# Performance work log

Measured on AMD Instinct MI355X. Metric: run time of the kernel, lower is better.

## Reference

```python
import jax, jax.numpy as jnp
import numpy as np

B, T, D, E = 4, 1024, 1024, 8
HD = 4 * D  # hdim = 4*dim


def setup_inputs() -> dict:
    key = jax.random.key(0)
    k1, k2, k3, k4 = jax.random.split(key, 4)
    std = 0.5 * D ** (-0.5)
    bound = (3.0 ** 0.5) * std
    x = jax.random.normal(k1, (B, T, D), dtype=jnp.float32)
    # router zero-init in source; use small random weights so routing is non-degenerate
    router_w = jax.random.normal(k2, (E, D), dtype=jnp.float32) * 0.02
    expert_fc = jax.random.uniform(k3, (E, D, HD), dtype=jnp.float32, minval=-bound, maxval=bound)
    # proj zero-init in source; use small random so output/backward are non-trivial
    expert_proj = jax.random.normal(k4, (E, D, HD), dtype=jnp.float32) * 0.02
    return {"x": x, "router_w": router_w, "expert_fc": expert_fc, "expert_proj": expert_proj}


def reference(x, router_w, expert_fc, expert_proj):
    # router: Linear(dim, E, bias=False) -> logits [B,T,E]
    logits = jnp.einsum('btd,ed->bte', x, router_w)
    probs = jax.nn.softmax(logits, axis=-1)
    expert_ids = jnp.argmax(probs, axis=-1)  # [B,T]; top-1 (max) routing
    # NOTE: source computes expert_weights (max prob) but does NOT use it in combine.
    mask = jax.nn.one_hot(expert_ids, E, dtype=x.dtype)  # [B,T,E]
    # Dense all-experts compute (faithful to source): h = x @ fc (F.linear with fc.T)
    h = jnp.einsum('btd,edh->ebth', x, expert_fc)
    h = jnp.square(jax.nn.relu(h))  # relu(h)**2
    # expert_output = h @ proj.T (F.linear with proj [dim, hdim])
    out_e = jnp.einsum('ebth,edh->ebtd', h, expert_proj)
    # masked combine: sum_e out_e * (ids == e)
    output = jnp.einsum('ebtd,bte->btd', out_e, mask)
    return output
```

## Files before the change

### kernel.cpp

```cpp
#include <hip/hip_runtime.h>
#include <hip/hip_bf16.h>
#include <stdint.h>

#define NE 8
#define DIM 1024
#define HDIM 4096
#define NTOK 4096
#define KSPLIT 4
#define MAXT 40

typedef unsigned short ushort_t;
typedef __attribute__((ext_vector_type(4))) float f32x4;
typedef __attribute__((ext_vector_type(8))) short bf16x8;
typedef __attribute__((ext_vector_type(8))) ushort_t u16x8;

#define WAITV4() asm volatile("s_waitcnt vmcnt(4)" ::: "memory")
#define WAITV6() asm volatile("s_waitcnt vmcnt(6)" ::: "memory")
#define WAITV0() asm volatile("s_waitcnt vmcnt(0)" ::: "memory")
#define WAITL0() asm volatile("s_waitcnt lgkmcnt(0)" ::: "memory")
#define SCHEDB() __builtin_amdgcn_sched_barrier(0)
#define BARRIER() __builtin_amdgcn_s_barrier()

__device__ __forceinline__ ushort_t f2b(float f) {
  union { float f; unsigned u; } c; c.f = f;
  unsigned u = c.u;
  return (ushort_t)((u + 0x7fffu + ((u >> 16) & 1u)) >> 16);
}

__device__ __forceinline__ unsigned pk2(float a, float b) {
  union { float f; unsigned u; } x, y; x.f = a; y.f = b;
  return __builtin_amdgcn_perm(y.u, x.u, 0x07060302);
}

__device__ __forceinline__ void gl2lds16(const void* g, void* l) {
  __builtin_amdgcn_global_load_lds(
      (__attribute__((address_space(1))) void*)g,
      (__attribute__((address_space(3))) void*)l, 16, 0, 0);
}

__global__ __launch_bounds__(256) void router_kernel(
    const float* __restrict__ x, const float* __restrict__ rw,
    int* __restrict__ eid, int* __restrict__ rank, int* __restrict__ cnt) {
  __shared__ float w[NE * 1028];
  for (int i = threadIdx.x; i < NE * DIM; i += 256) {
    int e = i >> 10, d = i & 1023;
    w[e * 1028 + d] = rw[i];
  }
  __syncthreads();
  int grp = threadIdx.x >> 3;
  int e = threadIdx.x & 7;
  int t = blockIdx.x * 32 + grp;
  const float4* xr = (const float4*)(x + (size_t)t * DIM);
  const float4* wr = (const float4*)(w + e * 1028);
  float acc = 0.f;
#pragma unroll 4
  for (int i = 0; i < DIM / 4; ++i) {
    float4 xv = xr[i], wv = wr[i];
    acc += xv.x * wv.x + xv.y * wv.y + xv.z * wv.z + xv.w * wv.w;
  }
  float v = acc; int ie = e;
#pragma unroll
  for (int m = 4; m; m >>= 1) {
    float ov = __shfl_xor(v, m, 8);
    int oi = __shfl_xor(ie, m, 8);
    if (ov > v || (ov == v && oi < ie)) { v = ov; ie = oi; }
  }
  if (e == 0) {
    eid[t] = ie;
    rank[t] = atomicAdd(&cnt[ie], 1);
  }
}

__global__ void scan_kernel(const int* __restrict__ cnt, int* __restrict__ offs,
                            int* __restrict__ tile_e, int* __restrict__ tile_m,
                            int* __restrict__ ntiles) {
  if (threadIdx.x == 0) {
    int s = 0, nt = 0;
    for (int e = 0; e < NE; ++e) {
      offs[e] = s;
      int c = cnt[e];
      for (int m = 0; m < c; m += 128) { tile_e[nt] = e; tile_m[nt] = m; ++nt; }
      s += c;
    }
    offs[NE] = s;
    *ntiles = nt;
  }
}

__global__ __launch_bounds__(256) void gather_kernel(
    const float* __restrict__ x, const int* __restrict__ eid,
    const int* __restrict__ rank, const int* __restrict__ offs,
    int* __restrict__ sorted, ushort_t* __restrict__ Xg) {
  int t = blockIdx.x;
  int e = eid[t];
  int pos = offs[e] + rank[t];
  if (threadIdx.x == 0) sorted[pos] = t;
  int i = threadIdx.x;
  float4 v = ((const float4*)(x + (size_t)t * DIM))[i];
  ushort4 o = make_ushort4(f2b(v.x), f2b(v.y), f2b(v.z), f2b(v.w));
  *(ushort4*)(Xg + (size_t)pos * DIM + i * 4) = o;
}

__global__ __launch_bounds__(256) void transpose_fc_kernel(
    const float* __restrict__ fc, ushort_t* __restrict__ fct) {
  __shared__ float tile[64][68];
  int e = blockIdx.z;
  int h0 = blockIdx.x * 64, d0 = blockIdx.y * 64;
  int tid = threadIdx.x;
  int rr = tid >> 4;
  int cc = (tid & 15) * 4;
  const float* src = fc + ((size_t)e * DIM + d0 + rr) * HDIM + h0 + cc;
#pragma unroll
  for (int i = 0; i < 4; ++i) {
    float4 v = *(const float4*)(src + (size_t)(i * 16) * HDIM);
    *(float4*)&tile[rr + i * 16][cc] = v;
  }
  __syncthreads();
  int hr = tid >> 2;
  int dseg = (tid & 3) * 16;
  union { ushort_t s[16]; u16x8 v[2]; } o;
#pragma unroll
  for (int j = 0; j < 16; ++j) o.s[j] = f2b(tile[dseg + j][hr]);
  ushort_t* dst = fct + ((size_t)e * HDIM + h0 + hr) * DIM + d0 + dseg;
  *(u16x8*)dst = o.v[0];
  *(u16x8*)(dst + 8) = o.v[1];
}

__global__ __launch_bounds__(256, 2) void gemm1_kernel(
    const ushort_t* __restrict__ Xg, const ushort_t* __restrict__ fct,
    const int* __restrict__ offs, const int* __restrict__ tile_e,
    const int* __restrict__ tile_m, const int* __restrict__ ntiles,
    ushort_t* __restrict__ H) {
  int lin = blockIdx.x + 32 * blockIdx.y;
  int sw = (lin & 7) * 160 + (lin >> 3);
  int bx = sw & 31, by = sw >> 5;

  if (by >= *ntiles) return;
  int e = tile_e[by];
  int mb = tile_m[by];
  int m0 = offs[e];
  int Me = offs[e + 1] - m0;
  int n0 = bx * 128;

  __shared__ ushort_t As[2][128 * 32];
  __shared__ ushort_t Bs[2][128 * 32];

  int tid = threadIdx.x;
  int wave = tid >> 6;
  int lane = tid & 63;

  const ushort_t* ap[2]; const ushort_t* bp[2];
  int soff[2];
#pragma unroll
  for (int q = 0; q < 2; ++q) {
    int rl = (wave * 2 + q) * 16 + (lane >> 2);
    int kc = (lane & 3) * 8;
    int rg = mb + rl; if (rg >= Me) rg = Me - 1;
    ap[q] = Xg + (size_t)(m0 + rg) * DIM + kc;
    bp[q] = fct + ((size_t)e * HDIM + n0 + rl) * DIM + kc;
    soff[q] = (wave * 2 + q) * 512;
  }

  f32x4 acc[4][4] = {};
  int wm = (wave & 1) * 64;
  int wn = (wave >> 1) * 64;
  int fr = lane & 15;
  int kq = (lane >> 4) * 8;

  auto stage = [&](int par, int tile) __attribute__((always_inline)) {
    int ko = tile * 32;
    gl2lds16(ap[0] + ko, &As[par][soff[0]]);
    gl2lds16(ap[1] + ko, &As[par][soff[1]]);
    gl2lds16(bp[0] + ko, &Bs[par][soff[0]]);
    gl2lds16(bp[1] + ko, &Bs[par][soff[1]]);
  };

  auto body = [&](int par, int t, bool issue) __attribute__((always_inline)) {
    BARRIER();
    SCHEDB();
    bf16x8 af[4], bf[4];
#pragma unroll
    for (int i = 0; i < 4; ++i) {
      af[i] = *(const bf16x8*)&As[par][(wm + i * 16 + fr) * 32 + kq];
      bf[i] = *(const bf16x8*)&Bs[par][(wn + i * 16 + fr) * 32 + kq];
    }
    WAITL0();
    SCHEDB();
    BARRIER();
    if (issue) stage(par, t + 2);
    __builtin_amdgcn_s_setprio(1);
#pragma unroll
    for (int i = 0; i < 4; ++i)
#pragma unroll
      for (int j = 0; j < 4; ++j)
        acc[i][j] = __builtin_amdgcn_mfma_f32_16x16x32_bf16(af[i], bf[j], acc[i][j], 0, 0, 0);
    __builtin_amdgcn_s_setprio(0);
  };

  stage(0, 0);
  stage(1, 1);
  for (int t = 0; t < 30; ++t) {
    WAITV4();
    body(t & 1, t, true);
  }
  WAITV4(); body(0, 30, false);
  WAITV0(); body(1, 31, false);

  int cq = (lane >> 4) * 4;
#pragma unroll
  for (int i = 0; i < 4; ++i) {
#pragma unroll
    for (int r = 0; r < 4; ++r) {
      int rl = wm + i * 16 + cq + r;
      int rg = mb + rl;
      if (rg < Me) {
        ushort_t* dst = H + (size_t)(m0 + rg) * HDIM + n0 + wn + (lane & 15);
#pragma unroll
        for (int j = 0; j < 4; ++j) {
          float v = acc[i][j][r];
          v = fmaxf(v, 0.f);
          dst[j * 16] = f2b(v * v);
        }
      }
    }
  }
}

__global__ __launch_bounds__(256, 2) void gemm2_kernel(
    const ushort_t* __restrict__ Hm, const float* __restrict__ pj,
    const int* __restrict__ offs, const int* __restrict__ tile_e,
    const int* __restrict__ tile_m, const int* __restrict__ ntiles,
    float* __restrict__ P) {
  int lin = blockIdx.x + 8 * (blockIdx.y + 40 * blockIdx.z);
  int sw = (lin & 7) * 160 + (lin >> 3);
  int bx = sw & 7, rem = sw >> 3;
  int by = rem % 40, bz = rem / 40;

  if (by >= *ntiles) return;
  int e = tile_e[by];
  int mb = tile_m[by];
  int ks = bz;
  int m0 = offs[e];
  int Me = offs[e + 1] - m0;
  int n0 = bx * 128;

  __shared__ ushort_t As[2][128 * 32];
  __shared__ ushort_t Bs[2][128 * 32];

  int tid = threadIdx.x;
  int wave = tid >> 6;
  int lane = tid & 63;

  int kbeg = ks * (HDIM / KSPLIT);

  const ushort_t* ap[2]; int soff[2];
#pragma unroll
  for (int q = 0; q < 2; ++q) {
    int rl = (wave * 2 + q) * 16 + (lane >> 2);
    int kc = (lane & 3) * 8;
    int rg = mb + rl; if (rg >= Me) rg = Me - 1;
    ap[q] = Hm + (size_t)(m0 + rg) * HDIM + kc + kbeg;
    soff[q] = (wave * 2 + q) * 512;
  }

  int br = tid >> 2;
  int bk = (tid & 3) * 8;
  const float* bsrc0 = pj + ((size_t)e * DIM + n0 + br) * HDIM + bk + kbeg;
  const float* bsrc1 = bsrc0 + (size_t)64 * HDIM;
  int boff0 = br * 32 + bk;
  int boff1 = (br + 64) * 32 + bk;

  f32x4 acc[4][4] = {};
  int wm = (wave & 1) * 64;
  int wn = (wave >> 1) * 64;
  int fr = lane & 15;
  int kq = (lane >> 4) * 8;

  auto stage = [&](int par, int tile, float4 (&bs)[4]) __attribute__((always_inline)) {
    int ko = tile * 32;
    bs[0] = *(const float4*)(bsrc0 + ko);
    bs[1] = *(const float4*)(bsrc0 + ko + 4);
    bs[2] = *(const float4*)(bsrc1 + ko);
    bs[3] = *(const float4*)(bsrc1 + ko + 4);
    gl2lds16(ap[0] + ko, &As[par][soff[0]]);
    gl2lds16(ap[1] + ko, &As[par][soff[1]]);
  };

  auto body = [&](int par, int t, bool issue, float4 (&bs)[4]) __attribute__((always_inline)) {
    union { unsigned u[4]; bf16x8 v; } w;
    w.u[0] = pk2(bs[0].x, bs[0].y); w.u[1] = pk2(bs[0].z, bs[0].w);
    w.u[2] = pk2(bs[1].x, bs[1].y); w.u[3] = pk2(bs[1].z, bs[1].w);
    *(bf16x8*)&Bs[par][boff0] = w.v;
    w.u[0] = pk2(bs[2].x, bs[2].y); w.u[1] = pk2(bs[2].z, bs[2].w);
    w.u[2] = pk2(bs[3].x, bs[3].y); w.u[3] = pk2(bs[3].z, bs[3].w);
    *(bf16x8*)&Bs[par][boff1] = w.v;
    WAITL0();
    BARRIER();
    SCHEDB();
    bf16x8 af[4], bf[4];
#pragma unroll
    for (int i = 0; i < 4; ++i) {
      af[i] = *(const bf16x8*)&As[par][(wm + i * 16 + fr) * 32 + kq];
      bf[i] = *(const bf16x8*)&Bs[par][(wn + i * 16 + fr) * 32 + kq];
    }
    WAITL0();
    SCHEDB();
    BARRIER();
    if (issue) stage(par, t + 2, bs);
    __builtin_amdgcn_s_setprio(1);
#pragma unroll
    for (int i = 0; i < 4; ++i)
#pragma unroll
      for (int j = 0; j < 4; ++j)
        acc[i][j] = __builtin_amdgcn_mfma_f32_16x16x32_bf16(af[i], bf[j], acc[i][j], 0, 0, 0);
    __builtin_amdgcn_s_setprio(0);
  };

  float4 bsA[4], bsB[4];
  stage(0, 0, bsA);
  stage(1, 1, bsB);
  for (int t = 0; t < 30; t += 2) {
    WAITV6();
    body(0, t, true, bsA);
    WAITV6();
    body(1, t + 1, true, bsB);
  }
  WAITV6(); body(0, 30, false, bsA);
  WAITV0(); body(1, 31, false, bsB);

  int cq = (lane >> 4) * 4;
#pragma unroll
  for (int i = 0; i < 4; ++i) {
#pragma unroll
    for (int r = 0; r < 4; ++r) {
      int rl = wm + i * 16 + cq + r;
      int rg = mb + rl;
      if (rg < Me) {
        float* dst = P + ((size_t)ks * NTOK + (m0 + rg)) * DIM + n0 + wn + (lane & 15);
#pragma unroll
        for (int j = 0; j < 4; ++j) dst[j * 16] = acc[i][j][r];
      }
    }
  }
}

__global__ __launch_bounds__(256) void reduce_kernel(
    const float* __restrict__ P, const int* __restrict__ sorted,
    float* __restrict__ out) {
  int pos = blockIdx.x;
  int tok = sorted[pos];
  int i = threadIdx.x;
  size_t base = (size_t)pos * DIM + i * 4;
  const size_t S = (size_t)NTOK * DIM;
  f32x4 s = *(const f32x4*)(P + base) + *(const f32x4*)(P + S + base) +
            *(const f32x4*)(P + 2 * S + base) + *(const f32x4*)(P + 3 * S + base);
  *(f32x4*)(out + (size_t)tok * DIM + i * 4) = s;
}

extern "C" void kernel_launch(void* const* d_in, const int* in_sizes, int n_in,
                              void* d_out, int out_size, void* d_ws, size_t ws_size,
                              hipStream_t stream) {
  const float* x  = (const float*)d_in[0];
  const float* rw = (const float*)d_in[1];
  const float* fc = (const float*)d_in[2];
  const float* pj = (const float*)d_in[3];
  float* out = (float*)d_out;
  char* ws = (char*)d_ws;

  int* eid        = (int*)(ws + 0x0000);
  int* rank       = (int*)(ws + 0x4000);
  int* cnt        = (int*)(ws + 0x8000);
  int* offs       = (int*)(ws + 0x8100);
  int* tile_e     = (int*)(ws + 0x8200);
  int* tile_m     = (int*)(ws + 0x8600);
  int* ntiles     = (int*)(ws + 0x8a00);
  int* sorted     = (int*)(ws + 0x9000);
  ushort_t* Xg    = (ushort_t*)(ws + 0x10000);
  ushort_t* H     = (ushort_t*)(ws + 0x810000);
  ushort_t* W     = (ushort_t*)(ws + 0x2810000);
  float* P        = (float*)W;

  hipMemsetAsync(cnt, 0, 32, stream);
  router_kernel<<<NTOK / 32, 256, 0, stream>>>(x, rw, eid, rank, cnt);
  scan_kernel<<<1, 64, 0, stream>>>(cnt, offs, tile_e, tile_m, ntiles);
  gather_kernel<<<NTOK, 256, 0, stream>>>(x, eid, rank, offs, sorted, Xg);
  transpose_fc_kernel<<<dim3(HDIM / 64, DIM / 64, NE), 256, 0, stream>>>(fc, W);
  gemm1_kernel<<<dim3(HDIM / 128, MAXT), 256, 0, stream>>>(Xg, W, offs, tile_e, tile_m, ntiles, H);
  gemm2_kernel<<<dim3(DIM / 128, MAXT, KSPLIT), 256, 0, stream>>>(H, pj, offs, tile_e, tile_m, ntiles, P);
  reduce_kernel<<<NTOK, 256, 0, stream>>>(P, sorted, out);
}
```

Baseline: 471.0 us.

## Enlarge grouped GEMM tiles to 256x256 with 8 waves and swizzled LDS

Both expert GEMMs move from 128x128x32 tiles with 4 waves to 256x256x64 tiles with 8 waves, each wave computing a 128x64 sub-tile. LDS rows are XOR-swizzled to avoid bank conflicts, and MFMA work is split into four phases interleaved with LDS fragment loads. The router scan now groups tokens into 256-row tiles, so fewer blocks are launched. This raises data reuse per global load, but padding waste per expert grows, fewer blocks run on the 256 CUs, and register and LDS pressure rise (64 KB of shared memory per block).

```diff
diff --git a/kernel.cpp b/kernel.cpp
--- a/kernel.cpp
+++ b/kernel.cpp
@@ -7,16 +7,15 @@
 #define HDIM 4096
 #define NTOK 4096
 #define KSPLIT 4
-#define MAXT 40
+#define MAXT 24
+#define NT 16
 
 typedef unsigned short ushort_t;
 typedef __attribute__((ext_vector_type(4))) float f32x4;
 typedef __attribute__((ext_vector_type(8))) short bf16x8;
 typedef __attribute__((ext_vector_type(8))) ushort_t u16x8;
 
-#define WAITV4() asm volatile("s_waitcnt vmcnt(4)" ::: "memory")
-#define WAITV6() asm volatile("s_waitcnt vmcnt(6)" ::: "memory")
-#define WAITV0() asm volatile("s_waitcnt vmcnt(0)" ::: "memory")
+#define WAITV(n) asm volatile("s_waitcnt vmcnt(" #n ")" ::: "memory")
 #define WAITL0() asm volatile("s_waitcnt lgkmcnt(0)" ::: "memory")
 #define SCHEDB() __builtin_amdgcn_sched_barrier(0)
 #define BARRIER() __builtin_amdgcn_s_barrier()
@@ -37,6 +36,37 @@
       (__attribute__((address_space(1))) void*)g,
       (__attribute__((address_space(3))) void*)l, 16, 0, 0);
 }
+
+#define PH_MFMA(mh, nh)                                                     \
+  { __builtin_amdgcn_s_setprio(1);                                          \
+    _Pragma("unroll")                                                       \
+    for (int i2 = 0; i2 < 4; ++i2) {                                        \
+      _Pragma("unroll")                                                     \
+      for (int j2 = 0; j2 < 2; ++j2) {                                      \
+        _Pragma("unroll")                                                   \
+        for (int kk = 0; kk < 2; ++kk)                                      \
+          acc[(mh)*4 + i2][(nh)*2 + j2] =                                   \
+            __builtin_amdgcn_mfma_f32_16x16x32_bf16(                        \
+              af[i2][kk], bf[(nh)*2 + j2][kk],                              \
+              acc[(mh)*4 + i2][(nh)*2 + j2], 0, 0, 0);                      \
+      }                                                                     \
+    }                                                                       \
+    __builtin_amdgcn_s_setprio(0); }
+
+#define LOAD_AF(mh)                                                         \
+  { _Pragma("unroll")                                                       \
+    for (int i2 = 0; i2 < 4; ++i2) {                                        \
+      _Pragma("unroll")                                                     \
+      for (int kk = 0; kk < 2; ++kk)                                        \
+        af[i2][kk] = *(const bf16x8*)&pA[aBase + ((mh)*64 + i2*16)*64 + ck[kk]]; \
+    } }
+#define LOAD_BF(nh)                                                         \
+  { _Pragma("unroll")                                                       \
+    for (int j2 = 0; j2 < 2; ++j2) {                                        \
+      _Pragma("unroll")                                                     \
+      for (int kk = 0; kk < 2; ++kk)                                        \
+        bf[(nh)*2 + j2][kk] = *(const bf16x8*)&pB[bBase + (((nh)*2 + j2)*16)*64 + ck[kk]]; \
+    } }
 
 __global__ __launch_bounds__(256) void router_kernel(
     const float* __restrict__ x, const float* __restrict__ rw,
@@ -79,7 +109,7 @@
     for (int e = 0; e < NE; ++e) {
       offs[e] = s;
       int c = cnt[e];
-      for (int m = 0; m < c; m += 128) { tile_e[nt] = e; tile_m[nt] = m; ++nt; }
+      for (int m = 0; m < c; m += 256) { tile_e[nt] = e; tile_m[nt] = m; ++nt; }
       s += c;
     }
     offs[NE] = s;
@@ -126,95 +156,92 @@
   *(u16x8*)(dst + 8) = o.v[1];
 }
 
-__global__ __launch_bounds__(256, 2) void gemm1_kernel(
+__global__ __launch_bounds__(512, 2) void gemm1_kernel(
     const ushort_t* __restrict__ Xg, const ushort_t* __restrict__ fct,
     const int* __restrict__ offs, const int* __restrict__ tile_e,
     const int* __restrict__ tile_m, const int* __restrict__ ntiles,
     ushort_t* __restrict__ H) {
-  int lin = blockIdx.x + 32 * blockIdx.y;
-  int sw = (lin & 7) * 160 + (lin >> 3);
-  int bx = sw & 31, by = sw >> 5;
-
+  __shared__ ushort_t As[2][16384];
+  __shared__ ushort_t Bs[2][16384];
+
+  int lin = blockIdx.x + 16 * blockIdx.y;
+  int sw = (lin & 7) * 48 + (lin >> 3);
+  int bx = sw & 15, by = sw >> 4;
   if (by >= *ntiles) return;
+
   int e = tile_e[by];
   int mb = tile_m[by];
   int m0 = offs[e];
   int Me = offs[e + 1] - m0;
-  int n0 = bx * 128;
-
-  __shared__ ushort_t As[2][128 * 32];
-  __shared__ ushort_t Bs[2][128 * 32];
+  int n0 = bx * 256;
 
   int tid = threadIdx.x;
   int wave = tid >> 6;
   int lane = tid & 63;
-
-  const ushort_t* ap[2]; const ushort_t* bp[2];
-  int soff[2];
-#pragma unroll
-  for (int q = 0; q < 2; ++q) {
-    int rl = (wave * 2 + q) * 16 + (lane >> 2);
-    int kc = (lane & 3) * 8;
-    int rg = mb + rl; if (rg >= Me) rg = Me - 1;
-    ap[q] = Xg + (size_t)(m0 + rg) * DIM + kc;
-    bp[q] = fct + ((size_t)e * HDIM + n0 + rl) * DIM + kc;
-    soff[q] = (wave * 2 + q) * 512;
-  }
-
-  f32x4 acc[4][4] = {};
-  int wm = (wave & 1) * 64;
-  int wn = (wave >> 1) * 64;
-  int fr = lane & 15;
-  int kq = (lane >> 4) * 8;
-
-  auto stage = [&](int par, int tile) __attribute__((always_inline)) {
-    int ko = tile * 32;
-    gl2lds16(ap[0] + ko, &As[par][soff[0]]);
-    gl2lds16(ap[1] + ko, &As[par][soff[1]]);
-    gl2lds16(bp[0] + ko, &Bs[par][soff[0]]);
-    gl2lds16(bp[1] + ko, &Bs[par][soff[1]]);
-  };
-
-  auto body = [&](int par, int t, bool issue) __attribute__((always_inline)) {
-    BARRIER();
-    SCHEDB();
-    bf16x8 af[4], bf[4];
-#pragma unroll
-    for (int i = 0; i < 4; ++i) {
-      af[i] = *(const bf16x8*)&As[par][(wm + i * 16 + fr) * 32 + kq];
-      bf[i] = *(const bf16x8*)&Bs[par][(wn + i * 16 + fr) * 32 + kq];
-    }
-    WAITL0();
-    SCHEDB();
-    BARRIER();
-    if (issue) stage(par, t + 2);
-    __builtin_amdgcn_s_setprio(1);
-#pragma unroll
-    for (int i = 0; i < 4; ++i)
-#pragma unroll
-      for (int j = 0; j < 4; ++j)
-        acc[i][j] = __builtin_amdgcn_mfma_f32_16x16x32_bf16(af[i], bf[j], acc[i][j], 0, 0, 0);
-    __builtin_amdgcn_s_setprio(0);
+  int fr = lane & 15, kq = lane >> 4;
+  int wr = wave & 1, wc = wave >> 1;
+
+  int swk = ((tid & 7) ^ ((tid >> 3) & 7)) * 8;
+  const ushort_t* aSrc[4]; const ushort_t* bSrc[4];
+#pragma unroll
+  for (int c = 0; c < 4; ++c) {
+    int r = c * 64 + (tid >> 3);
+    int rg = mb + r; if (rg >= Me) rg = Me - 1;
+    aSrc[c] = Xg + (size_t)(m0 + rg) * DIM + swk;
+    bSrc[c] = fct + ((size_t)e * HDIM + n0 + r) * DIM + swk;
+  }
+  int sdst = wave * 512;
+
+  int aBase = (wr * 128 + fr) * 64;
+  int bBase = (wc * 64 + fr) * 64;
+  int ck[2] = { (kq ^ (fr & 7)) * 8, ((4 + kq) ^ (fr & 7)) * 8 };
+
+  f32x4 acc[8][4] = {};
+  bf16x8 af[4][2], bf[4][2];
+
+  auto stage = [&](int p, int X) __attribute__((always_inline)) {
+    int ko = X * 64;
+#pragma unroll
+    for (int c = 0; c < 4; ++c)
+      gl2lds16(aSrc[c] + ko, &As[p][c * 4096 + sdst]);
+#pragma unroll
+    for (int c = 0; c < 4; ++c)
+      gl2lds16(bSrc[c] + ko, &Bs[p][c * 4096 + sdst]);
   };
 
   stage(0, 0);
   stage(1, 1);
-  for (int t = 0; t < 30; ++t) {
-    WAITV4();
-    body(t & 1, t, true);
-  }
-  WAITV4(); body(0, 30, false);
-  WAITV0(); body(1, 31, false);
-
-  int cq = (lane >> 4) * 4;
-#pragma unroll
-  for (int i = 0; i < 4; ++i) {
+  WAITV(8);
+
+  for (int T = 0; T < NT; ++T) {
+    const int p = T & 1;
+    const ushort_t* pA = As[p];
+    const ushort_t* pB = Bs[p];
+    BARRIER(); SCHEDB();
+    LOAD_AF(0); LOAD_BF(0);
+    WAITL0(); SCHEDB();
+    PH_MFMA(0, 0);
+    LOAD_BF(1);
+    WAITL0(); SCHEDB();
+    PH_MFMA(0, 1);
+    LOAD_AF(1);
+    WAITL0(); SCHEDB();
+    PH_MFMA(1, 0);
+    BARRIER(); SCHEDB();
+    if (T + 2 < NT) { stage(p, T + 2); WAITV(8); }
+    else if (T + 1 < NT) { WAITV(0); }
+    PH_MFMA(1, 1);
+  }
+
+  int cq = kq * 4;
+#pragma unroll
+  for (int i = 0; i < 8; ++i) {
 #pragma unroll
     for (int r = 0; r < 4; ++r) {
-      int rl = wm + i * 16 + cq + r;
+      int rl = wr * 128 + i * 16 + cq + r;
       int rg = mb + rl;
       if (rg < Me) {
-        ushort_t* dst = H + (size_t)(m0 + rg) * HDIM + n0 + wn + (lane & 15);
+        ushort_t* dst = H + (size_t)(m0 + rg) * HDIM + n0 + wc * 64 + fr;
 #pragma unroll
         for (int j = 0; j < 4; ++j) {
           float v = acc[i][j][r];
@@ -226,117 +253,120 @@
   }
 }
 
-__global__ __launch_bounds__(256, 2) void gemm2_kernel(
+__global__ __launch_bounds__(512, 2) void gemm2_kernel(
     const ushort_t* __restrict__ Hm, const float* __restrict__ pj,
     const int* __restrict__ offs, const int* __restrict__ tile_e,
     const int* __restrict__ tile_m, const int* __restrict__ ntiles,
     float* __restrict__ P) {
-  int lin = blockIdx.x + 8 * (blockIdx.y + 40 * blockIdx.z);
-  int sw = (lin & 7) * 160 + (lin >> 3);
-  int bx = sw & 7, rem = sw >> 3;
-  int by = rem % 40, bz = rem / 40;
-
+  __shared__ ushort_t As[2][16384];
+  __shared__ ushort_t Bs[2][16384];
+
+  int lin = blockIdx.x + 4 * (blockIdx.y + MAXT * blockIdx.z);
+  int sw = (lin & 7) * 48 + (lin >> 3);
+  int bx = sw & 3;
+  int t2 = sw >> 2;
+  int by = t2 % MAXT, bz = t2 / MAXT;
   if (by >= *ntiles) return;
+
   int e = tile_e[by];
   int mb = tile_m[by];
   int ks = bz;
   int m0 = offs[e];
   int Me = offs[e + 1] - m0;
-  int n0 = bx * 128;
-
-  __shared__ ushort_t As[2][128 * 32];
-  __shared__ ushort_t Bs[2][128 * 32];
+  int n0 = bx * 256;
+  int kbeg = ks * (HDIM / KSPLIT);
 
   int tid = threadIdx.x;
   int wave = tid >> 6;
   int lane = tid & 63;
-
-  int kbeg = ks * (HDIM / KSPLIT);
-
-  const ushort_t* ap[2]; int soff[2];
-#pragma unroll
-  for (int q = 0; q < 2; ++q) {
-    int rl = (wave * 2 + q) * 16 + (lane >> 2);
-    int kc = (lane & 3) * 8;
-    int rg = mb + rl; if (rg >= Me) rg = Me - 1;
-    ap[q] = Hm + (size_t)(m0 + rg) * HDIM + kc + kbeg;
-    soff[q] = (wave * 2 + q) * 512;
-  }
-
-  int br = tid >> 2;
-  int bk = (tid & 3) * 8;
-  const float* bsrc0 = pj + ((size_t)e * DIM + n0 + br) * HDIM + bk + kbeg;
-  const float* bsrc1 = bsrc0 + (size_t)64 * HDIM;
-  int boff0 = br * 32 + bk;
-  int boff1 = (br + 64) * 32 + bk;
-
-  f32x4 acc[4][4] = {};
-  int wm = (wave & 1) * 64;
-  int wn = (wave >> 1) * 64;
-  int fr = lane & 15;
-  int kq = (lane >> 4) * 8;
-
-  auto stage = [&](int par, int tile, float4 (&bs)[4]) __attribute__((always_inline)) {
-    int ko = tile * 32;
-    bs[0] = *(const float4*)(bsrc0 + ko);
-    bs[1] = *(const float4*)(bsrc0 + ko + 4);
-    bs[2] = *(const float4*)(bsrc1 + ko);
-    bs[3] = *(const float4*)(bsrc1 + ko + 4);
-    gl2lds16(ap[0] + ko, &As[par][soff[0]]);
-    gl2lds16(ap[1] + ko, &As[par][soff[1]]);
+  int fr = lane & 15, kq = lane >> 4;
+  int wr = wave & 1, wc = wave >> 1;
+
+  int swk = ((tid & 7) ^ ((tid >> 3) & 7)) * 8;
+  const ushort_t* aSrc[4];
+  const float* bSrc[4];
+  int bDst[4];
+#pragma unroll
+  for (int c = 0; c < 4; ++c) {
+    int r = c * 64 + (tid >> 3);
+    int rg = mb + r; if (rg >= Me) rg = Me - 1;
+    aSrc[c] = Hm + (size_t)(m0 + rg) * HDIM + kbeg + swk;
+    bSrc[c] = pj + ((size_t)e * DIM + n0 + r) * HDIM + kbeg + (tid & 7) * 8;
+    bDst[c] = r * 64 + swk;
+  }
+  int sdst = wave * 512;
+
+  int aBase = (wr * 128 + fr) * 64;
+  int bBase = (wc * 64 + fr) * 64;
+  int ck[2] = { (kq ^ (fr & 7)) * 8, ((4 + kq) ^ (fr & 7)) * 8 };
+
+  f32x4 acc[8][4] = {};
+  bf16x8 af[4][2], bf[4][2];
+  float4 bv[8];
+
+  auto loadB = [&](int X) __attribute__((always_inline)) {
+    int ko = X * 64;
+#pragma unroll
+    for (int c = 0; c < 4; ++c) {
+      bv[2 * c]     = *(const float4*)(bSrc[c] + ko);
+      bv[2 * c + 1] = *(const float4*)(bSrc[c] + ko + 4);
+    }
   };
-
-  auto body = [&](int par, int t, bool issue, float4 (&bs)[4]) __attribute__((always_inline)) {
-    union { unsigned u[4]; bf16x8 v; } w;
-    w.u[0] = pk2(bs[0].x, bs[0].y); w.u[1] = pk2(bs[0].z, bs[0].w);
-    w.u[2] = pk2(bs[1].x, bs[1].y); w.u[3] = pk2(bs[1].z, bs[1].w);
-    *(bf16x8*)&Bs[par][boff0] = w.v;
-    w.u[0] = pk2(bs[2].x, bs[2].y); w.u[1] = pk2(bs[2].z, bs[2].w);
-    w.u[2] = pk2(bs[3].x, bs[3].y); w.u[3] = pk2(bs[3].z, bs[3].w);
-    *(bf16x8*)&Bs[par][boff1] = w.v;
-    WAITL0();
-    BARRIER();
-    SCHEDB();
-    bf16x8 af[4], bf[4];
-#pragma unroll
-    for (int i = 0; i < 4; ++i) {
-      af[i] = *(const bf16x8*)&As[par][(wm + i * 16 + fr) * 32 + kq];
-      bf[i] = *(const bf16x8*)&Bs[par][(wn + i * 16 + fr) * 32 + kq];
+  auto writeB = [&](int pb) __attribute__((always_inline)) {
+#pragma unroll
+    for (int c = 0; c < 4; ++c) {
+      union { unsigned u[4]; bf16x8 v; } w;
+      w.u[0] = pk2(bv[2*c].x, bv[2*c].y);     w.u[1] = pk2(bv[2*c].z, bv[2*c].w);
+      w.u[2] = pk2(bv[2*c+1].x, bv[2*c+1].y); w.u[3] = pk2(bv[2*c+1].z, bv[2*c+1].w);
+      *(bf16x8*)&Bs[pb][bDst[c]] = w.v;
     }
-    WAITL0();
-    SCHEDB();
-    BARRIER();
-    if (issue) stage(par, t + 2, bs);
-    __builtin_amdgcn_s_setprio(1);
-#pragma unroll
-    for (int i = 0; i < 4; ++i)
-#pragma unroll
-      for (int j = 0; j < 4; ++j)
-        acc[i][j] = __builtin_amdgcn_mfma_f32_16x16x32_bf16(af[i], bf[j], acc[i][j], 0, 0, 0);
-    __builtin_amdgcn_s_setprio(0);
   };
-
-  float4 bsA[4], bsB[4];
-  stage(0, 0, bsA);
-  stage(1, 1, bsB);
-  for (int t = 0; t < 30; t += 2) {
-    WAITV6();
-    body(0, t, true, bsA);
-    WAITV6();
-    body(1, t + 1, true, bsB);
-  }
-  WAITV6(); body(0, 30, false, bsA);
-  WAITV0(); body(1, 31, false, bsB);
-
-  int cq = (lane >> 4) * 4;
-#pragma unroll
-  for (int i = 0; i < 4; ++i) {
+  auto stageA = [&](int p, int X) __attribute__((always_inline)) {
+    int ko = X * 64;
+#pragma unroll
+    for (int c = 0; c < 4; ++c)
+      gl2lds16(aSrc[c] + ko, &As[p][c * 4096 + sdst]);
+  };
+
+  loadB(0); stageA(0, 0);
+  WAITV(4);
+  writeB(0);
+  loadB(1); stageA(1, 1);
+  WAITV(4);
+  writeB(1);
+  WAITL0();
+
+  for (int T = 0; T < NT; ++T) {
+    const int p = T & 1;
+    const ushort_t* pA = As[p];
+    const ushort_t* pB = Bs[p];
+    BARRIER(); SCHEDB();
+    if (T >= 1 && T + 1 < NT) loadB(T + 1);
+    LOAD_AF(0); LOAD_BF(0);
+    WAITL0(); SCHEDB();
+    PH_MFMA(0, 0);
+    LOAD_BF(1);
+    WAITL0(); SCHEDB();
+    PH_MFMA(0, 1);
+    LOAD_AF(1);
+    WAITL0(); SCHEDB();
+    PH_MFMA(1, 0);
+    BARRIER(); SCHEDB();
+    if (T + 2 < NT) stageA(p, T + 2);
+    if (T + 1 < NT) { if (T + 2 < NT) { WAITV(4); } else { WAITV(0); } }
+    if (T >= 1 && T + 1 < NT) { writeB(p ^ 1); WAITL0(); }
+    PH_MFMA(1, 1);
+  }
+
+  int cq = kq * 4;
+#pragma unroll
+  for (int i = 0; i < 8; ++i) {
 #pragma unroll
     for (int r = 0; r < 4; ++r) {
-      int rl = wm + i * 16 + cq + r;
+      int rl = wr * 128 + i * 16 + cq + r;
       int rg = mb + rl;
       if (rg < Me) {
-        float* dst = P + ((size_t)ks * NTOK + (m0 + rg)) * DIM + n0 + wn + (lane & 15);
+        float* dst = P + ((size_t)ks * NTOK + (m0 + rg)) * DIM + n0 + wc * 64 + fr;
 #pragma unroll
         for (int j = 0; j < 4; ++j) dst[j * 16] = acc[i][j][r];
       }
@@ -385,7 +415,7 @@
   scan_kernel<<<1, 64, 0, stream>>>(cnt, offs, tile_e, tile_m, ntiles);
   gather_kernel<<<NTOK, 256, 0, stream>>>(x, eid, rank, offs, sorted, Xg);
   transpose_fc_kernel<<<dim3(HDIM / 64, DIM / 64, NE), 256, 0, stream>>>(fc, W);
-  gemm1_kernel<<<dim3(HDIM / 128, MAXT), 256, 0, stream>>>(Xg, W, offs, tile_e, tile_m, ntiles, H);
-  gemm2_kernel<<<dim3(DIM / 128, MAXT, KSPLIT), 256, 0, stream>>>(H, pj, offs, tile_e, tile_m, ntiles, P);
+  gemm1_kernel<<<dim3(HDIM / 256, MAXT), 512, 0, stream>>>(Xg, W, offs, tile_e, tile_m, ntiles, H);
+  gemm2_kernel<<<dim3(DIM / 256, MAXT, KSPLIT), 512, 0, stream>>>(H, pj, offs, tile_e, tile_m, ntiles, P);
   reduce_kernel<<<NTOK, 256, 0, stream>>>(P, sorted, out);
 }
```

Result: slower. 498.6 us (+5.9%).
